# Performance work log

Measured on AMD Instinct MI355X. Metric: run time of the kernel, lower is better.

## Reference

```python
import jax, jax.numpy as jnp
import numpy as np

N = 50000
E = 1600000
F = 128
G = 64  # number of graphs in the batch


def gat_layer(x, src, dst, W, a_src, a_dst, bias, heads, out_dim, concat):
    n = x.shape[0]
    h = (x @ W).reshape(n, heads, out_dim)                      # [N,H,D]
    alpha_src = jnp.sum(h * a_src, axis=-1)                     # [N,H]
    alpha_dst = jnp.sum(h * a_dst, axis=-1)                     # [N,H]
    e = jax.nn.leaky_relu(alpha_src[src] + alpha_dst[dst], negative_slope=0.2)  # [E,H]
    # segment softmax over edges grouped by destination node
    m = jax.ops.segment_max(e, dst, num_segments=n)
    m = jnp.where(jnp.isfinite(m), m, 0.0)
    ex = jnp.exp(e - m[dst])
    denom = jax.ops.segment_sum(ex, dst, num_segments=n)
    alpha = ex / (denom[dst] + 1e-16)                           # [E,H]
    msg = h[src] * alpha[:, :, None]                            # [E,H,D]
    out = jax.ops.segment_sum(msg, dst, num_segments=n)         # [N,H,D]
    if concat:
        out = out.reshape(n, heads * out_dim)
    else:
        out = out.mean(axis=1)
    return out + bias


def setup_inputs() -> dict:
    key = jax.random.key(0)
    ks = jax.random.split(key, 12)
    x = jax.random.normal(ks[0], (N, F), dtype=jnp.float32)
    edge_index = jax.random.randint(ks[1], (2, E), 0, N, dtype=jnp.int32)
    batch = jnp.sort(jax.random.randint(ks[2], (N,), 0, G, dtype=jnp.int32))
    s = 0.1
    W1 = jax.random.normal(ks[3], (F, 4 * 32), dtype=jnp.float32) * s
    a_src1 = jax.random.normal(ks[4], (4, 32), dtype=jnp.float32) * s
    a_dst1 = jax.random.normal(ks[5], (4, 32), dtype=jnp.float32) * s
    b1 = jnp.zeros((4 * 32,), dtype=jnp.float32)
    W2 = jax.random.normal(ks[6], (4 * 32, 2 * 16), dtype=jnp.float32) * s
    a_src2 = jax.random.normal(ks[7], (2, 16), dtype=jnp.float32) * s
    a_dst2 = jax.random.normal(ks[8], (2, 16), dtype=jnp.float32) * s
    b2 = jnp.zeros((16,), dtype=jnp.float32)
    fcW = jax.random.normal(ks[9], (16, 1), dtype=jnp.float32) * s
    fcb = jnp.zeros((1,), dtype=jnp.float32)
    return {"x": x, "edge_index": edge_index, "batch": batch,
            "W1": W1, "a_src1": a_src1, "a_dst1": a_dst1, "b1": b1,
            "W2": W2, "a_src2": a_src2, "a_dst2": a_dst2, "b2": b2,
            "fcW": fcW, "fcb": fcb}


def reference(x, edge_index, batch, W1, a_src1, a_dst1, b1, W2, a_src2, a_dst2, b2, fcW, fcb):
    n = x.shape[0]
    # PyG GATConv default: add self loops
    loops = jnp.arange(n, dtype=edge_index.dtype)
    src = jnp.concatenate([edge_index[0], loops])
    dst = jnp.concatenate([edge_index[1], loops])
    # eval mode: dropouts are no-ops
    h = jax.nn.relu(gat_layer(x, src, dst, W1, a_src1, a_dst1, b1, 4, 32, True))
    h = gat_layer(h, src, dst, W2, a_src2, a_dst2, b2, 2, 16, False)
    # global mean pool over graphs
    sums = jax.ops.segment_sum(h, batch, num_segments=G)        # [G,16]
    counts = jax.ops.segment_sum(jnp.ones((n,), h.dtype), batch, num_segments=G)
    pooled = sums / jnp.maximum(counts, 1.0)[:, None]
    return pooled @ fcW + fcb                                   # [G,1]
```

## Files before the change

### kernel.cpp

```cpp
#include <hip/hip_runtime.h>

#define LRELU(x) ((x) > 0.f ? (x) : 0.2f*(x))
typedef unsigned int uint;

__device__ inline unsigned short f2bf(float f) {
    union { float f; unsigned u; } v; v.f = f;
    unsigned r = v.u + 0x7FFF + ((v.u >> 16) & 1);
    return (unsigned short)(r >> 16);
}
__device__ inline uint packbf(float a, float b) {
    return (uint)f2bf(a) | ((uint)f2bf(b) << 16);
}
__device__ inline float bflo(uint u){ union{uint u; float f;}v; v.u = u<<16; return v.f; }
__device__ inline float bfhi(uint u){ union{uint u; float f;}v; v.u = u & 0xFFFF0000u; return v.f; }
__device__ inline float f4get(const float4& v, int i) {
    return i==0 ? v.x : i==1 ? v.y : i==2 ? v.z : v.w;
}


#define CSR_SHIFT 7
#define CSR_NBLK  512

__global__ __launch_bounds__(256) void bucket_count_kernel(
    const int* __restrict__ dst, int E, int chunk, int nb,
    int* __restrict__ blockCntT)
{
    __shared__ int cnt[1024];
    int t = threadIdx.x, k = blockIdx.x;
    for (int i = t; i < nb; i += 256) cnt[i] = 0;
    __syncthreads();
    int e0 = k * chunk, e1 = min(e0 + chunk, E);
    for (int e = e0 + t; e < e1; e += 256)
        atomicAdd(&cnt[dst[e] >> CSR_SHIFT], 1);
    __syncthreads();
    for (int b = t; b < nb; b += 256)
        blockCntT[b * CSR_NBLK + k] = cnt[b];
}

__global__ __launch_bounds__(512) void row_scan_kernel(
    int* __restrict__ blockCntT, int* __restrict__ tot)
{
    __shared__ int sm[512];
    int b = blockIdx.x, t = threadIdx.x;
    int* row = blockCntT + b * CSR_NBLK;
    int v = row[t];
    sm[t] = v;
    __syncthreads();
    for (int off = 1; off < 512; off <<= 1) {
        int u = (t >= off) ? sm[t - off] : 0;
        __syncthreads(); sm[t] += u; __syncthreads();
    }
    row[t] = sm[t] - v;
    if (t == 511) tot[b] = sm[511];
}

__global__ __launch_bounds__(1024) void total_scan_kernel(
    const int* __restrict__ tot, int nb, int* __restrict__ bucketBase)
{
    __shared__ int sm[1024];
    int t = threadIdx.x;
    int v = (t < nb) ? tot[t] : 0;
    sm[t] = v;
    __syncthreads();
    for (int off = 1; off < 1024; off <<= 1) {
        int u = (t >= off) ? sm[t - off] : 0;
        __syncthreads(); sm[t] += u; __syncthreads();
    }
    if (t < nb) bucketBase[t] = sm[t] - v;
    if (t == 1023) bucketBase[nb] = sm[1023];
}

__global__ __launch_bounds__(256) void bucket_scatter_kernel(
    const int* __restrict__ src, const int* __restrict__ dst, int E, int chunk, int nb,
    const int* __restrict__ blockCntT, const int* __restrict__ bucketBase,
    uint* __restrict__ ebuf)
{
    __shared__ int cur[1024];
    int t = threadIdx.x, k = blockIdx.x;
    for (int b = t; b < nb; b += 256)
        cur[b] = bucketBase[b] + blockCntT[b * CSR_NBLK + k];
    __syncthreads();
    int e0 = k * chunk, e1 = min(e0 + chunk, E);
    for (int e = e0 + t; e < e1; e += 256) {
        int d = dst[e], s_ = src[e];
        int pos = atomicAdd(&cur[d >> CSR_SHIFT], 1);
        ebuf[pos] = ((uint)s_ << 7) | (uint)(d & 127);
    }
}

__global__ __launch_bounds__(256) void local_csr_kernel(
    const uint* __restrict__ ebuf, const int* __restrict__ bucketBase,
    int n, int E, int* __restrict__ rowptr, int* __restrict__ csr)
{
    __shared__ int lbase[1 << CSR_SHIFT];
    __shared__ int lcur[1 << CSR_SHIFT];
    __shared__ int ldeg[1 << CSR_SHIFT];
    int b = blockIdx.x, t = threadIdx.x;
    int n0 = b << CSR_SHIFT;
    int base = bucketBase[b], end = bucketBase[b + 1];
    if (t < (1 << CSR_SHIFT)) ldeg[t] = 0;
    __syncthreads();
    for (int e = base + t; e < end; e += 256)
        atomicAdd(&ldeg[ebuf[e] & 127], 1);
    __syncthreads();
    if (t == 0) {
        int run = base;
        for (int i = 0; i < (1 << CSR_SHIFT); ++i) {
            lbase[i] = run; lcur[i] = run; run += ldeg[i];
        }
    }
    __syncthreads();
    int node = n0 + t;
    if (t < (1 << CSR_SHIFT) && node < n) rowptr[node] = lbase[t];
    if (b == 0 && t == 0) rowptr[n] = E;
    for (int e = base + t; e < end; e += 256) {
        uint ed = ebuf[e];
        int pos = atomicAdd(&lcur[ed & 127], 1);
        csr[pos] = (int)(ed >> 7);
    }
}


template<int COLS, int HEADS>
__global__ __launch_bounds__(256) void gemm_alpha_kernel(
    const float* __restrict__ x, const float* __restrict__ W,
    const float* __restrict__ a_src, const float* __restrict__ a_dst,
    uint* __restrict__ hq, float* __restrict__ as_out,
    float* __restrict__ ad_out, int n)
{
    constexpr int K = 128;
    constexpr int CPT = COLS / 8;
    constexpr int NPT = 4;
    constexpr int DIM = COLS / HEADS;
    constexpr int TPH = DIM / CPT;
    constexpr int NSLOT = COLS / 4;
    __shared__ float4 WL[K * NSLOT];

    int t = threadIdx.x;
    for (int idx = t * 4; idx < K * COLS; idx += 1024) {
        float4 w = *(const float4*)(W + idx);
        int k = idx / COLS, c = idx % COLS;
        int slot = c >> 2;
        if (COLS == 128) slot = (slot >> 2) | ((slot & 3) << 3);
        WL[k * NSLOT + slot] = w;
    }
    __syncthreads();

    int m_ = t & 7;
    int node0 = blockIdx.x * (32 * NPT) + (t >> 3) * NPT;
    if (node0 >= n) return;
    int c0 = m_ * CPT;

    const float* xr[NPT];
#pragma unroll
    for (int i = 0; i < NPT; i++) xr[i] = x + (size_t)min(node0 + i, n - 1) * K;

    float acc[NPT][CPT];
#pragma unroll
    for (int i = 0; i < NPT; i++)
#pragma unroll
        for (int q = 0; q < CPT; q++) acc[i][q] = 0.f;

    for (int k4 = 0; k4 < K; k4 += 4) {
        float4 xv[NPT];
#pragma unroll
        for (int i = 0; i < NPT; i++) xv[i] = *(const float4*)(xr[i] + k4);
#pragma unroll
        for (int kk = 0; kk < 4; kk++) {
#pragma unroll
            for (int j = 0; j < CPT / 4; j++) {
                int slot = (COLS == 128) ? (m_ | (j << 3)) : m_;
                float4 w = WL[(k4 + kk) * NSLOT + slot];
#pragma unroll
                for (int i = 0; i < NPT; i++) {
                    float xa = f4get(xv[i], kk);
                    acc[i][j*4+0] += xa * w.x;
                    acc[i][j*4+1] += xa * w.y;
                    acc[i][j*4+2] += xa * w.z;
                    acc[i][j*4+3] += xa * w.w;
                }
            }
        }
    }

    int head = c0 / DIM, lc = c0 - head * DIM;
    float asc[CPT], adc[CPT];
#pragma unroll
    for (int q = 0; q < CPT; q++) {
        asc[q] = a_src[head * DIM + lc + q];
        adc[q] = a_dst[head * DIM + lc + q];
    }

#pragma unroll
    for (int i = 0; i < NPT; i++) {
        int node = node0 + i;
        if (node >= n) break;
        if constexpr (COLS == 128) {
            uint wds[4];
#pragma unroll
            for (int j = 0; j < 4; j++) {
                int u = 0;
                u = __builtin_amdgcn_cvt_pk_fp8_f32(acc[i][j*4+0], acc[i][j*4+1], u, false);
                u = __builtin_amdgcn_cvt_pk_fp8_f32(acc[i][j*4+2], acc[i][j*4+3], u, true);
                wds[j] = (uint)u;
            }
            *(uint4*)(hq + (size_t)node * 32 + m_ * 4) = make_uint4(wds[0], wds[1], wds[2], wds[3]);
        } else {
            uint w0 = packbf(acc[i][0], acc[i][1]);
            uint w1 = packbf(acc[i][2], acc[i][3]);
            *(uint2*)(hq + (size_t)node * 16 + m_ * 2) = make_uint2(w0, w1);
        }
        float ps = 0.f, pd = 0.f;
#pragma unroll
        for (int q = 0; q < CPT; q++) {
            ps += acc[i][q] * asc[q];
            pd += acc[i][q] * adc[q];
        }
#pragma unroll
        for (int off = 1; off < TPH; off <<= 1) {
            ps += __shfl_xor(ps, off);
            pd += __shfl_xor(pd, off);
        }
        if ((m_ & (TPH - 1)) == 0) {
            as_out[node * HEADS + head] = ps;
            ad_out[node * HEADS + head] = pd;
        }
    }
}


__global__ __launch_bounds__(256) void agg1_kernel(
    const float4* __restrict__ as1, const float4* __restrict__ ad1,
    const uint* __restrict__ h1q, const int* __restrict__ rowptr,
    const int* __restrict__ csr, const float* __restrict__ b1,
    float* __restrict__ hout, int n)
{
    __shared__ int   sIdx[4][64];
    __shared__ float sEx[4][64][4];
    __shared__ int   mxch;

    int t = threadIdx.x;
    int w = t >> 6, tw = t & 63;
    int g = tw >> 3, l = tw & 7;
    int head = l >> 1;
    int node = blockIdx.x * 4 + w;
    if (t == 0) mxch = 0;
    bool valid = node < n;
    int nv = valid ? node : 0;

    float4 adv = ad1[nv];
    int rp = rowptr[nv], re = valid ? rowptr[nv + 1] : rp;
    __syncthreads();
    if (tw == 0) atomicMax(&mxch, (re - rp + 63) >> 6);
    __syncthreads();
    int mx = mxch;

    float acc[16];
#pragma unroll
    for (int i = 0; i < 16; i++) acc[i] = 0.f;
    float den = 0.f;

    for (int c = 0; c < mx; ++c) {
        int base = rp + c * 64;
        int cnt = min(64, re - base);
        if (tw < cnt) {
            int s = csr[base + tw];
            sIdx[w][tw] = s;
            float4 av = as1[s];
            sEx[w][tw][0] = __expf(LRELU(av.x + adv.x));
            sEx[w][tw][1] = __expf(LRELU(av.y + adv.y));
            sEx[w][tw][2] = __expf(LRELU(av.z + adv.z));
            sEx[w][tw][3] = __expf(LRELU(av.w + adv.w));
        }
        __syncthreads();
#pragma unroll 2
        for (int e = g; e < cnt; e += 8) {
            int s = sIdx[w][e];
            float ex = sEx[w][e][head];
            den += ex;
            uint4 u = *(const uint4*)(h1q + ((size_t)s << 5) + (l << 2));
            uint ua[4] = {u.x, u.y, u.z, u.w};
#pragma unroll
            for (int j = 0; j < 4; j++) {
                auto p0 = __builtin_amdgcn_cvt_pk_f32_fp8(ua[j], false);
                auto p1 = __builtin_amdgcn_cvt_pk_f32_fp8(ua[j], true);
                acc[j*4+0] += ex * p0[0]; acc[j*4+1] += ex * p0[1];
                acc[j*4+2] += ex * p1[0]; acc[j*4+3] += ex * p1[1];
            }
        }
        __syncthreads();
    }

#pragma unroll
    for (int i = 0; i < 16; i++) {
        acc[i] += __shfl_xor(acc[i], 8);
        acc[i] += __shfl_xor(acc[i], 16);
        acc[i] += __shfl_xor(acc[i], 32);
    }
    den += __shfl_xor(den, 8);
    den += __shfl_xor(den, 16);
    den += __shfl_xor(den, 32);

    if (valid) {
        float4 asv = as1[node];
        float ex = __expf(LRELU(f4get(asv, head) + f4get(adv, head)));
        den += ex;
        uint4 u = *(const uint4*)(h1q + ((size_t)node << 5) + (l << 2));
        uint ua[4] = {u.x, u.y, u.z, u.w};
#pragma unroll
        for (int j = 0; j < 4; j++) {
            auto p0 = __builtin_amdgcn_cvt_pk_f32_fp8(ua[j], false);
            auto p1 = __builtin_amdgcn_cvt_pk_f32_fp8(ua[j], true);
            acc[j*4+0] += ex * p0[0]; acc[j*4+1] += ex * p0[1];
            acc[j*4+2] += ex * p1[0]; acc[j*4+3] += ex * p1[1];
        }
        if (g == 0) {
            float inv = 1.f / (den + 1e-16f);
            const float4* b4 = (const float4*)b1;
#pragma unroll
            for (int j = 0; j < 4; j++) {
                float4 bv = b4[(l << 2) + j];
                float4 o;
                o.x = fmaxf(acc[j*4+0] * inv + bv.x, 0.f);
                o.y = fmaxf(acc[j*4+1] * inv + bv.y, 0.f);
                o.z = fmaxf(acc[j*4+2] * inv + bv.z, 0.f);
                o.w = fmaxf(acc[j*4+3] * inv + bv.w, 0.f);
                ((float4*)hout)[(size_t)node * 32 + (l << 2) + j] = o;
            }
        }
    }
}


__global__ __launch_bounds__(256) void agg2_kernel(
    const float2* __restrict__ as2, const float2* __restrict__ ad2,
    const uint* __restrict__ h2q, const int* __restrict__ rowptr,
    const int* __restrict__ csr, const float* __restrict__ b2,
    float* __restrict__ hf, int n)
{
    __shared__ int   sIdx[4][64];
    __shared__ float sEx[4][64][2];
    __shared__ int   mxch;

    int t = threadIdx.x;
    int w = t >> 6, tw = t & 63;
    int g = tw >> 3, l = tw & 7;
    int head = l >> 2;
    int node = blockIdx.x * 4 + w;
    if (t == 0) mxch = 0;
    bool valid = node < n;
    int nv = valid ? node : 0;

    float2 adv = ad2[nv];
    float adh = head ? adv.y : adv.x;
    int rp = rowptr[nv], re = valid ? rowptr[nv + 1] : rp;
    __syncthreads();
    if (tw == 0) atomicMax(&mxch, (re - rp + 63) >> 6);
    __syncthreads();
    int mx = mxch;

    float acc[4] = {0.f, 0.f, 0.f, 0.f};
    float den = 0.f;

    for (int c = 0; c < mx; ++c) {
        int base = rp + c * 64;
        int cnt = min(64, re - base);
        if (tw < cnt) {
            int s = csr[base + tw];
            sIdx[w][tw] = s;
            float2 av = as2[s];
            sEx[w][tw][0] = __expf(LRELU(av.x + adv.x));
            sEx[w][tw][1] = __expf(LRELU(av.y + adv.y));
        }
        __syncthreads();
#pragma unroll 2
        for (int e = g; e < cnt; e += 8) {
            int s = sIdx[w][e];
            float ex = sEx[w][e][head];
            den += ex;
            uint2 u = *(const uint2*)(h2q + ((size_t)s << 4) + (l << 1));
            acc[0] += ex * bflo(u.x); acc[1] += ex * bfhi(u.x);
            acc[2] += ex * bflo(u.y); acc[3] += ex * bfhi(u.y);
        }
        __syncthreads();
    }

#pragma unroll
    for (int i = 0; i < 4; i++) {
        acc[i] += __shfl_xor(acc[i], 8);
        acc[i] += __shfl_xor(acc[i], 16);
        acc[i] += __shfl_xor(acc[i], 32);
    }
    den += __shfl_xor(den, 8);
    den += __shfl_xor(den, 16);
    den += __shfl_xor(den, 32);

    if (valid) {
        float2 asv = as2[node];
        float ash = head ? asv.y : asv.x;
        float ex = __expf(LRELU(ash + adh));
        den += ex;
        uint2 u = *(const uint2*)(h2q + ((size_t)node << 4) + (l << 1));
        acc[0] += ex * bflo(u.x); acc[1] += ex * bfhi(u.x);
        acc[2] += ex * bflo(u.y); acc[3] += ex * bfhi(u.y);

        float inv = 1.f / (den + 1e-16f);
        float v0 = acc[0] * inv, v1 = acc[1] * inv, v2 = acc[2] * inv, v3 = acc[3] * inv;
        float o0 = 0.5f * (v0 + __shfl_xor(v0, 4));
        float o1 = 0.5f * (v1 + __shfl_xor(v1, 4));
        float o2 = 0.5f * (v2 + __shfl_xor(v2, 4));
        float o3 = 0.5f * (v3 + __shfl_xor(v3, 4));
        if (g == 0 && l < 4) {
            float4 o;
            o.x = o0 + b2[4*l+0]; o.y = o1 + b2[4*l+1];
            o.z = o2 + b2[4*l+2]; o.w = o3 + b2[4*l+3];
            *(float4*)(hf + (size_t)node * 16 + 4 * l) = o;
        }
    }
}


__global__ __launch_bounds__(256) void pool_kernel(
    const float* __restrict__ hf, const int* __restrict__ batch,
    float* __restrict__ sums, float* __restrict__ counts, int n)
{
    int t = threadIdx.x;
    int d = t & 15, j = t >> 4;
    int base = blockIdx.x * 256 + j * 16;
    float run = 0.f, cnt = 0.f;
    int cg = -1;
    for (int i = 0; i < 16; ++i) {
        int nn = base + i;
        if (nn >= n) break;
        int g = batch[nn];
        if (g != cg) {
            if (cg >= 0) { atomicAdd(&sums[cg * 16 + d], run); if (d == 0) atomicAdd(&counts[cg], cnt); }
            cg = g; run = 0.f; cnt = 0.f;
        }
        run += hf[(size_t)nn * 16 + d];
        cnt += 1.f;
    }
    if (cg >= 0) { atomicAdd(&sums[cg * 16 + d], run); if (d == 0) atomicAdd(&counts[cg], cnt); }
}

__global__ void final_kernel(const float* __restrict__ sums, const float* __restrict__ counts,
                             const float* __restrict__ fcW, const float* __restrict__ fcb,
                             float* __restrict__ out, int G)
{
    int g = blockIdx.x * 64 + threadIdx.x;
    if (g < G) {
        float c = fmaxf(counts[g], 1.f);
        float s = 0.f;
        for (int dd = 0; dd < 16; ++dd) s += (sums[g * 16 + dd] / c) * fcW[dd];
        out[g] = s + fcb[0];
    }
}


extern "C" void kernel_launch(void* const* d_in, const int* in_sizes, int n_in,
                              void* d_out, int out_size, void* d_ws, size_t ws_size,
                              hipStream_t stream)
{
    const float* x      = (const float*)d_in[0];
    const int*   ei     = (const int*)d_in[1];
    const int*   batch  = (const int*)d_in[2];
    const float* W1     = (const float*)d_in[3];
    const float* a_src1 = (const float*)d_in[4];
    const float* a_dst1 = (const float*)d_in[5];
    const float* b1     = (const float*)d_in[6];
    const float* W2     = (const float*)d_in[7];
    const float* a_src2 = (const float*)d_in[8];
    const float* a_dst2 = (const float*)d_in[9];
    const float* b2     = (const float*)d_in[10];
    const float* fcW    = (const float*)d_in[11];
    const float* fcb    = (const float*)d_in[12];
    float* out = (float*)d_out;

    int n = in_sizes[0] / 128;
    int E = in_sizes[1] / 2;
    int G = out_size;
    const int* srcA = ei;
    const int* dstA = ei + E;

    int nb = (n + (1 << CSR_SHIFT) - 1) >> CSR_SHIFT;
    int chunk = (E + CSR_NBLK - 1) / CSR_NBLK;

    char* p = (char*)d_ws;
    auto alloc = [&](size_t bytes) { char* r = p; p += (bytes + 255) & ~(size_t)255; return r; };
    int*   blockCntT  = (int*)alloc((size_t)nb * CSR_NBLK * 4);
    int*   tot        = (int*)alloc((size_t)nb * 4);
    int*   bucketBase = (int*)alloc((size_t)(nb + 1) * 4);
    int*   rowptr     = (int*)alloc((size_t)(n + 1) * 4);
    int*   csr        = (int*)alloc((size_t)E * 4);
    uint*  h1q        = (uint*)alloc((size_t)n * 32 * 4);
    float* as1        = (float*)alloc((size_t)n * 16);
    float* ad1        = (float*)alloc((size_t)n * 16);
    float* hrelu      = (float*)alloc((size_t)n * 128 * 4);
    uint*  h2q        = (uint*)alloc((size_t)n * 16 * 4);
    float* as2        = (float*)alloc((size_t)n * 8);
    float* ad2        = (float*)alloc((size_t)n * 8);
    float* hf         = (float*)alloc((size_t)n * 16 * 4);
    float* sums       = (float*)alloc((size_t)G * 16 * 4 + (size_t)G * 4);
    float* counts     = sums + G * 16;

    uint* ebuf = (uint*)hrelu;

    hipMemsetAsync(sums, 0, (size_t)G * 16 * 4 + (size_t)G * 4, stream);

    bucket_count_kernel<<<CSR_NBLK, 256, 0, stream>>>(dstA, E, chunk, nb, blockCntT);
    row_scan_kernel<<<nb, 512, 0, stream>>>(blockCntT, tot);
    total_scan_kernel<<<1, 1024, 0, stream>>>(tot, nb, bucketBase);
    bucket_scatter_kernel<<<CSR_NBLK, 256, 0, stream>>>(srcA, dstA, E, chunk, nb,
                                                        blockCntT, bucketBase, ebuf);
    local_csr_kernel<<<nb, 256, 0, stream>>>(ebuf, bucketBase, n, E, rowptr, csr);

    int gb = (n + 127) / 128;
    gemm_alpha_kernel<128, 4><<<gb, 256, 0, stream>>>(x, W1, a_src1, a_dst1, h1q, as1, ad1, n);
    agg1_kernel<<<(n + 3) / 4, 256, 0, stream>>>((const float4*)as1, (const float4*)ad1,
                                                 h1q, rowptr, csr, b1, hrelu, n);
    gemm_alpha_kernel<32, 2><<<gb, 256, 0, stream>>>(hrelu, W2, a_src2, a_dst2, h2q, as2, ad2, n);
    agg2_kernel<<<(n + 3) / 4, 256, 0, stream>>>((const float2*)as2, (const float2*)ad2,
                                                 h2q, rowptr, csr, b2, hf, n);
    pool_kernel<<<(n + 255) / 256, 256, 0, stream>>>(hf, batch, sums, counts, n);
    final_kernel<<<1, 64, 0, stream>>>(sums, counts, fcW, fcb, out, G);
}
```

Baseline: 209.3 us.

## Drop shared-memory staging and block syncs in GAT aggregation kernels

Both aggregation kernels no longer stage neighbor indices and exp scores in shared memory behind block-wide barriers and a shared max-chunk atomic. Each wave now walks its own CSR row directly, loading the index and per-head source score and computing the exponent per edge, then exits early when its node is out of range. This removes __syncthreads and the block-level coupling that made every wave wait on the longest row. In exchange, the csr index and score loads, plus the exp, are repeated by every lane of each edge group rather than done once per edge and shared.

```diff
diff --git a/kernel.cpp b/kernel.cpp
--- a/kernel.cpp
+++ b/kernel.cpp
@@ -230,82 +230,33 @@
 
 
 __global__ __launch_bounds__(256) void agg1_kernel(
-    const float4* __restrict__ as1, const float4* __restrict__ ad1,
+    const float* __restrict__ as1f, const float* __restrict__ ad1f,
     const uint* __restrict__ h1q, const int* __restrict__ rowptr,
     const int* __restrict__ csr, const float* __restrict__ b1,
     float* __restrict__ hout, int n)
 {
-    __shared__ int   sIdx[4][64];
-    __shared__ float sEx[4][64][4];
-    __shared__ int   mxch;
-
     int t = threadIdx.x;
     int w = t >> 6, tw = t & 63;
     int g = tw >> 3, l = tw & 7;
     int head = l >> 1;
     int node = blockIdx.x * 4 + w;
-    if (t == 0) mxch = 0;
-    bool valid = node < n;
-    int nv = valid ? node : 0;
-
-    float4 adv = ad1[nv];
-    int rp = rowptr[nv], re = valid ? rowptr[nv + 1] : rp;
-    __syncthreads();
-    if (tw == 0) atomicMax(&mxch, (re - rp + 63) >> 6);
-    __syncthreads();
-    int mx = mxch;
+    if (node >= n) return;
+
+    float adh = ad1f[node * 4 + head];
+    int rp = rowptr[node], re = rowptr[node + 1];
 
     float acc[16];
 #pragma unroll
     for (int i = 0; i < 16; i++) acc[i] = 0.f;
     float den = 0.f;
 
-    for (int c = 0; c < mx; ++c) {
-        int base = rp + c * 64;
-        int cnt = min(64, re - base);
-        if (tw < cnt) {
-            int s = csr[base + tw];
-            sIdx[w][tw] = s;
-            float4 av = as1[s];
-            sEx[w][tw][0] = __expf(LRELU(av.x + adv.x));
-            sEx[w][tw][1] = __expf(LRELU(av.y + adv.y));
-            sEx[w][tw][2] = __expf(LRELU(av.z + adv.z));
-            sEx[w][tw][3] = __expf(LRELU(av.w + adv.w));
-        }
-        __syncthreads();
 #pragma unroll 2
-        for (int e = g; e < cnt; e += 8) {
-            int s = sIdx[w][e];
-            float ex = sEx[w][e][head];
-            den += ex;
-            uint4 u = *(const uint4*)(h1q + ((size_t)s << 5) + (l << 2));
-            uint ua[4] = {u.x, u.y, u.z, u.w};
-#pragma unroll
-            for (int j = 0; j < 4; j++) {
-                auto p0 = __builtin_amdgcn_cvt_pk_f32_fp8(ua[j], false);
-                auto p1 = __builtin_amdgcn_cvt_pk_f32_fp8(ua[j], true);
-                acc[j*4+0] += ex * p0[0]; acc[j*4+1] += ex * p0[1];
-                acc[j*4+2] += ex * p1[0]; acc[j*4+3] += ex * p1[1];
-            }
-        }
-        __syncthreads();
-    }
-
-#pragma unroll
-    for (int i = 0; i < 16; i++) {
-        acc[i] += __shfl_xor(acc[i], 8);
-        acc[i] += __shfl_xor(acc[i], 16);
-        acc[i] += __shfl_xor(acc[i], 32);
-    }
-    den += __shfl_xor(den, 8);
-    den += __shfl_xor(den, 16);
-    den += __shfl_xor(den, 32);
-
-    if (valid) {
-        float4 asv = as1[node];
-        float ex = __expf(LRELU(f4get(asv, head) + f4get(adv, head)));
+    for (int e = rp + g; e < re; e += 8) {
+        int s = csr[e];
+        float a = as1f[s * 4 + head];
+        uint4 u = *(const uint4*)(h1q + ((size_t)s << 5) + (l << 2));
+        float ex = __expf(LRELU(a + adh));
         den += ex;
-        uint4 u = *(const uint4*)(h1q + ((size_t)node << 5) + (l << 2));
         uint ua[4] = {u.x, u.y, u.z, u.w};
 #pragma unroll
         for (int j = 0; j < 4; j++) {
@@ -314,75 +265,87 @@
             acc[j*4+0] += ex * p0[0]; acc[j*4+1] += ex * p0[1];
             acc[j*4+2] += ex * p1[0]; acc[j*4+3] += ex * p1[1];
         }
-        if (g == 0) {
-            float inv = 1.f / (den + 1e-16f);
-            const float4* b4 = (const float4*)b1;
-#pragma unroll
-            for (int j = 0; j < 4; j++) {
-                float4 bv = b4[(l << 2) + j];
-                float4 o;
-                o.x = fmaxf(acc[j*4+0] * inv + bv.x, 0.f);
-                o.y = fmaxf(acc[j*4+1] * inv + bv.y, 0.f);
-                o.z = fmaxf(acc[j*4+2] * inv + bv.z, 0.f);
-                o.w = fmaxf(acc[j*4+3] * inv + bv.w, 0.f);
-                ((float4*)hout)[(size_t)node * 32 + (l << 2) + j] = o;
-            }
+    }
+
+    if (g == 0) {
+        float a = as1f[node * 4 + head];
+        float ex = __expf(LRELU(a + adh));
+        den += ex;
+        uint4 u = *(const uint4*)(h1q + ((size_t)node << 5) + (l << 2));
+        uint ua[4] = {u.x, u.y, u.z, u.w};
+#pragma unroll
+        for (int j = 0; j < 4; j++) {
+            auto p0 = __builtin_amdgcn_cvt_pk_f32_fp8(ua[j], false);
+            auto p1 = __builtin_amdgcn_cvt_pk_f32_fp8(ua[j], true);
+            acc[j*4+0] += ex * p0[0]; acc[j*4+1] += ex * p0[1];
+            acc[j*4+2] += ex * p1[0]; acc[j*4+3] += ex * p1[1];
+        }
+    }
+
+#pragma unroll
+    for (int i = 0; i < 16; i++) {
+        acc[i] += __shfl_xor(acc[i], 8);
+        acc[i] += __shfl_xor(acc[i], 16);
+        acc[i] += __shfl_xor(acc[i], 32);
+    }
+    den += __shfl_xor(den, 8);
+    den += __shfl_xor(den, 16);
+    den += __shfl_xor(den, 32);
+
+    if (g == 0) {
+        float inv = 1.f / (den + 1e-16f);
+        const float4* b4 = (const float4*)b1;
+#pragma unroll
+        for (int j = 0; j < 4; j++) {
+            float4 bv = b4[(l << 2) + j];
+            float4 o;
+            o.x = fmaxf(acc[j*4+0] * inv + bv.x, 0.f);
+            o.y = fmaxf(acc[j*4+1] * inv + bv.y, 0.f);
+            o.z = fmaxf(acc[j*4+2] * inv + bv.z, 0.f);
+            o.w = fmaxf(acc[j*4+3] * inv + bv.w, 0.f);
+            ((float4*)hout)[(size_t)node * 32 + (l << 2) + j] = o;
         }
     }
 }
 
 
 __global__ __launch_bounds__(256) void agg2_kernel(
-    const float2* __restrict__ as2, const float2* __restrict__ ad2,
+    const float* __restrict__ as2f, const float* __restrict__ ad2f,
     const uint* __restrict__ h2q, const int* __restrict__ rowptr,
     const int* __restrict__ csr, const float* __restrict__ b2,
     float* __restrict__ hf, int n)
 {
-    __shared__ int   sIdx[4][64];
-    __shared__ float sEx[4][64][2];
-    __shared__ int   mxch;
-
     int t = threadIdx.x;
     int w = t >> 6, tw = t & 63;
     int g = tw >> 3, l = tw & 7;
     int head = l >> 2;
     int node = blockIdx.x * 4 + w;
-    if (t == 0) mxch = 0;
-    bool valid = node < n;
-    int nv = valid ? node : 0;
-
-    float2 adv = ad2[nv];
-    float adh = head ? adv.y : adv.x;
-    int rp = rowptr[nv], re = valid ? rowptr[nv + 1] : rp;
-    __syncthreads();
-    if (tw == 0) atomicMax(&mxch, (re - rp + 63) >> 6);
-    __syncthreads();
-    int mx = mxch;
+    if (node >= n) return;
+
+    float adh = ad2f[node * 2 + head];
+    int rp = rowptr[node], re = rowptr[node + 1];
 
     float acc[4] = {0.f, 0.f, 0.f, 0.f};
     float den = 0.f;
 
-    for (int c = 0; c < mx; ++c) {
-        int base = rp + c * 64;
-        int cnt = min(64, re - base);
-        if (tw < cnt) {
-            int s = csr[base + tw];
-            sIdx[w][tw] = s;
-            float2 av = as2[s];
-            sEx[w][tw][0] = __expf(LRELU(av.x + adv.x));
-            sEx[w][tw][1] = __expf(LRELU(av.y + adv.y));
-        }
-        __syncthreads();
 #pragma unroll 2
-        for (int e = g; e < cnt; e += 8) {
-            int s = sIdx[w][e];
-            float ex = sEx[w][e][head];
-            den += ex;
-            uint2 u = *(const uint2*)(h2q + ((size_t)s << 4) + (l << 1));
-            acc[0] += ex * bflo(u.x); acc[1] += ex * bfhi(u.x);
-            acc[2] += ex * bflo(u.y); acc[3] += ex * bfhi(u.y);
-        }
-        __syncthreads();
+    for (int e = rp + g; e < re; e += 8) {
+        int s = csr[e];
+        float a = as2f[s * 2 + head];
+        uint2 u = *(const uint2*)(h2q + ((size_t)s << 4) + (l << 1));
+        float ex = __expf(LRELU(a + adh));
+        den += ex;
+        acc[0] += ex * bflo(u.x); acc[1] += ex * bfhi(u.x);
+        acc[2] += ex * bflo(u.y); acc[3] += ex * bfhi(u.y);
+    }
+
+    if (g == 0) {
+        float a = as2f[node * 2 + head];
+        float ex = __expf(LRELU(a + adh));
+        den += ex;
+        uint2 u = *(const uint2*)(h2q + ((size_t)node << 4) + (l << 1));
+        acc[0] += ex * bflo(u.x); acc[1] += ex * bfhi(u.x);
+        acc[2] += ex * bflo(u.y); acc[3] += ex * bfhi(u.y);
     }
 
 #pragma unroll
@@ -395,27 +358,17 @@
     den += __shfl_xor(den, 16);
     den += __shfl_xor(den, 32);
 
-    if (valid) {
-        float2 asv = as2[node];
-        float ash = head ? asv.y : asv.x;
-        float ex = __expf(LRELU(ash + adh));
-        den += ex;
-        uint2 u = *(const uint2*)(h2q + ((size_t)node << 4) + (l << 1));
-        acc[0] += ex * bflo(u.x); acc[1] += ex * bfhi(u.x);
-        acc[2] += ex * bflo(u.y); acc[3] += ex * bfhi(u.y);
-
-        float inv = 1.f / (den + 1e-16f);
-        float v0 = acc[0] * inv, v1 = acc[1] * inv, v2 = acc[2] * inv, v3 = acc[3] * inv;
-        float o0 = 0.5f * (v0 + __shfl_xor(v0, 4));
-        float o1 = 0.5f * (v1 + __shfl_xor(v1, 4));
-        float o2 = 0.5f * (v2 + __shfl_xor(v2, 4));
-        float o3 = 0.5f * (v3 + __shfl_xor(v3, 4));
-        if (g == 0 && l < 4) {
-            float4 o;
-            o.x = o0 + b2[4*l+0]; o.y = o1 + b2[4*l+1];
-            o.z = o2 + b2[4*l+2]; o.w = o3 + b2[4*l+3];
-            *(float4*)(hf + (size_t)node * 16 + 4 * l) = o;
-        }
+    float inv = 1.f / (den + 1e-16f);
+    float v0 = acc[0] * inv, v1 = acc[1] * inv, v2 = acc[2] * inv, v3 = acc[3] * inv;
+    float o0 = 0.5f * (v0 + __shfl_xor(v0, 4));
+    float o1 = 0.5f * (v1 + __shfl_xor(v1, 4));
+    float o2 = 0.5f * (v2 + __shfl_xor(v2, 4));
+    float o3 = 0.5f * (v3 + __shfl_xor(v3, 4));
+    if (g == 0 && l < 4) {
+        float4 o;
+        o.x = o0 + b2[4*l+0]; o.y = o1 + b2[4*l+1];
+        o.z = o2 + b2[4*l+2]; o.w = o3 + b2[4*l+3];
+        *(float4*)(hf + (size_t)node * 16 + 4 * l) = o;
     }
 }
 
@@ -516,11 +469,9 @@
 
     int gb = (n + 127) / 128;
     gemm_alpha_kernel<128, 4><<<gb, 256, 0, stream>>>(x, W1, a_src1, a_dst1, h1q, as1, ad1, n);
-    agg1_kernel<<<(n + 3) / 4, 256, 0, stream>>>((const float4*)as1, (const float4*)ad1,
-                                                 h1q, rowptr, csr, b1, hrelu, n);
+    agg1_kernel<<<(n + 3) / 4, 256, 0, stream>>>(as1, ad1, h1q, rowptr, csr, b1, hrelu, n);
     gemm_alpha_kernel<32, 2><<<gb, 256, 0, stream>>>(hrelu, W2, a_src2, a_dst2, h2q, as2, ad2, n);
-    agg2_kernel<<<(n + 3) / 4, 256, 0, stream>>>((const float2*)as2, (const float2*)ad2,
-                                                 h2q, rowptr, csr, b2, hf, n);
+    agg2_kernel<<<(n + 3) / 4, 256, 0, stream>>>(as2, ad2, h2q, rowptr, csr, b2, hf, n);
     pool_kernel<<<(n + 255) / 256, 256, 0, stream>>>(hf, batch, sums, counts, n);
     final_kernel<<<1, 64, 0, stream>>>(sums, counts, fcW, fcb, out, G);
 }
```

Result: faster. 195.9 us (-6.4%).
